# Kernel tuning notes

Measured on AMD Instinct MI355X. Metric: run time of the kernel, lower is better.

## Reference

```python
import jax, jax.numpy as jnp
import numpy as np

LMAX = 8                         # lmax-1 used by s2/so3 irreps
DIMS = [2 * l + 1 for l in range(LMAX + 1)]
S2_OFF = np.cumsum([0] + DIMS).tolist()            # offsets into 81-dim s2 irreps
SO3_OFF = np.cumsum([0] + [d * d for d in DIMS]).tolist()  # offsets into 969-dim so3 irreps
S2_DIM = S2_OFF[-1]              # 81
SO3_DIM = SO3_OFF[-1]            # 969
F_IN = 81                        # multiplicity into S2Conv
F_SO3 = 300
C = 768                          # encoder feature channels
KS = 7                           # encoder feature map / kernel size
B = 8
G_S2 = 48                        # s2 healpix grid rec_level=1
G_ACT = 4096                     # SO3Activation grid points (stand-in for res=20 grid)
G_SO3 = 36864                    # so3 healpix grid rec_level=3


def setup_inputs() -> dict:
    key = jax.random.key(0)
    ks = jax.random.split(key, 7)
    return {
        "x": jax.random.normal(ks[0], (B, C, KS, KS), jnp.float32),
        "F": jax.random.normal(ks[1], (F_IN, S2_DIM * C, KS, KS), jnp.float32) * 0.02,
        "w_s2": jax.random.normal(ks[2], (F_IN, F_SO3, G_S2), jnp.float32) * 0.1,
        "Y": jax.random.normal(ks[3], (G_S2, S2_DIM), jnp.float32),
        "w_so3": jax.random.normal(ks[4], (F_SO3, 1, G_SO3), jnp.float32) * 0.1,
        "D": jax.random.normal(ks[5], (G_SO3, SO3_DIM), jnp.float32),
        "D_act": jax.random.normal(ks[6], (G_ACT, SO3_DIM), jnp.float32),
    }


def _forward(x, F, w_s2, Y, w_so3, D, D_act):
    b = x.shape[0]
    # ---- Induction layer: split expanded R2Conv filter into 768-channel chunks,
    # stack, contract with feature map. g_split: (n=81, c_out=81, C, 7, 7)
    g = jnp.swapaxes(F.reshape(F_IN, S2_DIM, C, KS, KS), 0, 1)
    y = jnp.einsum('ijkhw,akhw->aji', g, x)          # (B, 81, 81): (batch, f_in, s2 irreps)

    # ---- S2Conv: expand kernel into irrep space, per-l block linear (s2 -> so3 irreps)
    psi = jnp.einsum('ni,xyn->xyi', Y, w_s2) / np.sqrt(G_S2)  # (81, 300, 81)
    outs = []
    for l, d in enumerate(DIMS):
        o = S2_OFF[l]
        xl = y[:, :, o:o + d]                        # (B, f_in, 2l+1)
        wl = psi[:, :, o:o + d]                      # (f_in, f_out, mul_out=2l+1)
        ol = jnp.einsum('bfm,fgu->bgum', xl, wl) / np.sqrt(F_IN)
        outs.append(ol.reshape(b, F_SO3, d * d))
    z = jnp.concatenate(outs, axis=-1)               # (B, 300, 969)

    # ---- SO3Activation: to grid, relu, back to irreps
    s = jnp.einsum('bfi,gi->bfg', z, D_act)
    z = jnp.einsum('bfg,gi->bfi', jax.nn.relu(s), D_act) / G_ACT

    # ---- SO3Conv: expand kernel via Wigner-D buffer, per-l block linear (so3 -> so3)
    psi2 = jnp.einsum('ni,xyn->xyi', D, w_so3) / np.sqrt(G_SO3)  # (300, 1, 969)
    outs = []
    for l, d in enumerate(DIMS):
        o = SO3_OFF[l]
        xl = z[:, :, o:o + d * d].reshape(b, F_SO3, d, d)   # (B, f, u, m)
        wl = psi2[:, :, o:o + d * d].reshape(F_SO3, 1, d, d)  # (f, g, v, u)
        ol = jnp.einsum('bfum,fgvu->bgvm', xl, wl) / np.sqrt(F_SO3 * d)
        outs.append(ol.reshape(b, 1, d * d))
    return jnp.concatenate(outs, axis=-1)            # (B, 1, 969)


def reference(x, F, w_s2, Y, w_so3, D, D_act):
    return _forward(x, F, w_s2, Y, w_so3, D, D_act)
```

## Files before the change

kernel.cpp:

```cpp
#include <hip/hip_runtime.h>
#include <hip/hip_bf16.h>
#include <math.h>

#define THREADS 256

constexpr int B_    = 8;
constexpr int C_    = 768;
constexpr int KS_   = 7;
constexpr int F_IN  = 81;
constexpr int F_SO3 = 300;
constexpr int S2_DIM  = 81;
constexpr int SO3_DIM = 969;
constexpr int G_S2  = 48;
constexpr int G_ACT = 4096;
constexpr int G_SO3 = 36864;
constexpr int CKK   = C_ * KS_ * KS_;
constexpr int CKK4  = CKK / 4;
constexpr int NPAIR = F_IN * S2_DIM;

constexpr int D2_SPLIT = 4;
constexpr int E1_SPLIT = 16;
constexpr int F_SPLIT  = 5;

__constant__ int d_S2_OFF[10]  = {0, 1, 4, 9, 16, 25, 36, 49, 64, 81};
__constant__ int d_SO3_OFF[10] = {0, 1, 10, 35, 84, 165, 286, 455, 680, 969};

struct CEnt { unsigned char u, m, so, l; };
struct CLut { CEnt v[992]; };
constexpr CLut make_clut() {
  CLut t{};
  int S2O[10]  = {0, 1, 4, 9, 16, 25, 36, 49, 64, 81};
  int SO3O[10] = {0, 1, 10, 35, 84, 165, 286, 455, 680, 969};
  for (int i = 0; i < 969; ++i) {
    int l = 0;
    while (i >= SO3O[l + 1]) ++l;
    int d = 2 * l + 1, r = i - SO3O[l];
    t.v[i].u  = (unsigned char)(r / d);
    t.v[i].m  = (unsigned char)(r % d);
    t.v[i].so = (unsigned char)S2O[l];
    t.v[i].l  = (unsigned char)l;
  }
  return t;
}
__constant__ CLut g_clut = make_clut();

using short8 = __attribute__((ext_vector_type(8))) short;
using f32x4  = __attribute__((ext_vector_type(4))) float;
using f4v    = __attribute__((ext_vector_type(4))) float;

#define GL16(gp, lp)                                                        \
  __builtin_amdgcn_global_load_lds(                                         \
      (const __attribute__((address_space(1))) void*)(gp),                  \
      (__attribute__((address_space(3))) void*)(lp), 16, 0, 0)

constexpr size_t AL(size_t x) { return (x + 1023) & ~(size_t)1023; }
constexpr size_t O_Y     = 0;
constexpr size_t O_PSI   = O_Y     + AL((size_t)8 * NPAIR * 4);
constexpr size_t O_ZBF   = O_PSI   + AL((size_t)F_IN * F_SO3 * 81 * 4);
constexpr size_t O_DACT  = O_ZBF   + AL((size_t)2432 * 1024 * 2);
constexpr size_t O_DACTT = O_DACT  + AL((size_t)4096 * 1024 * 2);
constexpr size_t O_WSO3  = O_DACTT + AL((size_t)1024 * 4096 * 2);
constexpr size_t O_DT    = O_WSO3  + AL((size_t)384 * 36864 * 2);
constexpr size_t O_SBF   = O_DT    + AL((size_t)1024 * 36864 * 2);
constexpr size_t O_D2P   = O_SBF   + AL((size_t)2432 * 4096 * 2);
constexpr size_t O_E1P   = O_D2P   + AL((size_t)D2_SPLIT * 2432 * 1024 * 4);
constexpr size_t O_PSI2  = O_E1P   + AL((size_t)E1_SPLIT * 384 * 1024 * 4);
constexpr size_t O_SFP   = O_PSI2  + AL((size_t)F_SO3 * SO3_DIM * 4);
constexpr size_t FAST_NEED = O_SFP + AL((size_t)F_SPLIT * 8 * SO3_DIM * 4);

constexpr size_t WS_Y    = 0;
constexpr size_t WS_PSI  = 52488;
constexpr size_t WS_Z    = 2020788;
constexpr size_t WS_S    = 4346388;
constexpr size_t WS_Z2   = 14176788;
constexpr size_t WS_P2P  = 16502388;
constexpr size_t WS_PSI2 = 18827988;

__global__ __launch_bounds__(THREADS, 4) void k_stage_a3(
    const float* __restrict__ Fm, const float* __restrict__ x, float* __restrict__ y) {
  const int p0  = blockIdx.x * 3;
  const int tid = threadIdx.x;
  const f4v* __restrict__ F4 = (const f4v*)Fm;
  const f4v* __restrict__ x4 = (const f4v*)x;

  float acc[3][8];
#pragma unroll
  for (int p = 0; p < 3; ++p)
#pragma unroll
    for (int b = 0; b < 8; ++b) acc[p][b] = 0.f;

  int i = tid;
  for (int it = 0; it < 18; ++it, i += 2 * THREADS) {
    f4v xv0[8], xv1[8];
#pragma unroll
    for (int b = 0; b < 8; ++b) {
      xv0[b] = x4[b * CKK4 + i];
      xv1[b] = x4[b * CKK4 + i + THREADS];
    }
#pragma unroll
    for (int p = 0; p < 3; ++p) {
      f4v fv0 = __builtin_nontemporal_load(&F4[(size_t)(p0 + p) * CKK4 + i]);
      f4v fv1 = __builtin_nontemporal_load(&F4[(size_t)(p0 + p) * CKK4 + i + THREADS]);
#pragma unroll
      for (int b = 0; b < 8; ++b) {
        acc[p][b] += fv0[0] * xv0[b][0] + fv0[1] * xv0[b][1] + fv0[2] * xv0[b][2] + fv0[3] * xv0[b][3];
        acc[p][b] += fv1[0] * xv1[b][0] + fv1[1] * xv1[b][1] + fv1[2] * xv1[b][2] + fv1[3] * xv1[b][3];
      }
    }
  }
  if (i < CKK4) {
    f4v xv0[8];
#pragma unroll
    for (int b = 0; b < 8; ++b) xv0[b] = x4[b * CKK4 + i];
#pragma unroll
    for (int p = 0; p < 3; ++p) {
      f4v fv0 = __builtin_nontemporal_load(&F4[(size_t)(p0 + p) * CKK4 + i]);
#pragma unroll
      for (int b = 0; b < 8; ++b)
        acc[p][b] += fv0[0] * xv0[b][0] + fv0[1] * xv0[b][1] + fv0[2] * xv0[b][2] + fv0[3] * xv0[b][3];
    }
  }

  __shared__ float red[4][24];
  const int lane = tid & 63, wid = tid >> 6;
#pragma unroll
  for (int p = 0; p < 3; ++p) {
#pragma unroll
    for (int b = 0; b < 8; ++b) {
      float v = acc[p][b];
      v += __shfl_down(v, 32);
      v += __shfl_down(v, 16);
      v += __shfl_down(v, 8);
      v += __shfl_down(v, 4);
      v += __shfl_down(v, 2);
      v += __shfl_down(v, 1);
      if (lane == 0) red[wid][p * 8 + b] = v;
    }
  }
  __syncthreads();
  if (tid < 24) {
    float v = red[0][tid] + red[1][tid] + red[2][tid] + red[3][tid];
    int p = tid / 8, b = tid % 8;
    y[(size_t)b * NPAIR + p0 + p] = v;
  }
}

__device__ __forceinline__ void cvt4_body(const float* __restrict__ src,
                                          __hip_bfloat16* __restrict__ dst,
                                          int R, int Cs, int Cp, int blk) {
  size_t e0 = ((size_t)blk * THREADS + threadIdx.x) * 4;
  int r = (int)(e0 / (unsigned)Cp), c = (int)(e0 % (unsigned)Cp);
  __hip_bfloat16 o[4];
#pragma unroll
  for (int j = 0; j < 4; ++j) {
    float v = (r < R && c + j < Cs) ? src[(size_t)r * Cs + c + j] : 0.f;
    o[j] = __float2bfloat16(v);
  }
  *(ushort4*)(&dst[e0]) = *(const ushort4*)o;
}

__device__ __forceinline__ void tr_body(const float* __restrict__ src,
                                        __hip_bfloat16* __restrict__ dst,
                                        int R, int Cs, size_t dstStride, int bx, int by,
                                        char* smemc) {
  float (*tile)[33] = (float(*)[33])smemc;
  const int c0 = bx * 32, r0 = by * 32;
  const int tx = threadIdx.x & 31, ty = threadIdx.x >> 5;
#pragma unroll
  for (int i = 0; i < 32; i += 8) {
    int r = r0 + ty + i, c = c0 + tx;
    tile[ty + i][tx] = (c < Cs) ? src[(size_t)r * Cs + c] : 0.f;
  }
  __syncthreads();
  const int rp = threadIdx.x & 15;
  const int cl = threadIdx.x >> 4;
#pragma unroll
  for (int j = 0; j < 2; ++j) {
    int cc = cl + 16 * j;
    int c  = c0 + cc;
    if (c < Cs) {
      __hip_bfloat16 o[2];
      o[0] = __float2bfloat16(tile[2 * rp][cc]);
      o[1] = __float2bfloat16(tile[2 * rp + 1][cc]);
      *(ushort2*)(&dst[(size_t)c * dstStride + r0 + 2 * rp]) = *(const ushort2*)o;
    }
  }
}

__device__ __forceinline__ void psi_body(const float* __restrict__ w_s2,
                                         const float* __restrict__ Y,
                                         float* __restrict__ psi_t, int blk) {
  int idx = blk * THREADS + threadIdx.x;
  if (idx >= F_IN * F_SO3 * S2_DIM) return;
  int s  = idx % S2_DIM;
  int t1 = idx / S2_DIM;
  int f  = t1 % F_IN;
  int g  = t1 / F_IN;
  const float* w = w_s2 + ((size_t)f * F_SO3 + g) * G_S2;
  float acc = 0.f;
#pragma unroll 8
  for (int n = 0; n < G_S2; ++n) acc += w[n] * Y[n * S2_DIM + s];
  psi_t[idx] = acc * 0.14433756729740643f;
}

constexpr int UB1 = 4096;
constexpr int UB2 = 3968;
constexpr int UB3 = 13824;
constexpr int UB4 = 35712;
constexpr int UB5 = 7689;
constexpr int UB_TOT = UB1 + UB2 + UB3 + UB4 + UB5;

__global__ __launch_bounds__(THREADS) void k_uber(
    const float* __restrict__ D_act, __hip_bfloat16* __restrict__ Dact_bf,
    __hip_bfloat16* __restrict__ DactT_bf,
    const float* __restrict__ w_so3, __hip_bfloat16* __restrict__ wso3_bf,
    const float* __restrict__ D, __hip_bfloat16* __restrict__ DT_bf,
    const float* __restrict__ w_s2, const float* __restrict__ Y, float* __restrict__ psi_t) {
  __shared__ __align__(16) char smem[4352];
  int b = blockIdx.x;
  if (b < UB1) { cvt4_body(D_act, Dact_bf, G_ACT, SO3_DIM, 1024, b); return; }
  b -= UB1;
  if (b < UB2) { tr_body(D_act, DactT_bf, G_ACT, SO3_DIM, 4096, b % 31, b / 31, smem); return; }
  b -= UB2;
  if (b < UB3) { cvt4_body(w_so3, wso3_bf, F_SO3, G_SO3, G_SO3, b); return; }
  b -= UB3;
  if (b < UB4) { tr_body(D, DT_bf, G_SO3, SO3_DIM, 36864, b % 31, b / 31, smem); return; }
  b -= UB4;
  psi_body(w_s2, Y, psi_t, b);
}

__global__ __launch_bounds__(THREADS) void k_stage_c_bf(
    const float* __restrict__ y, const float* __restrict__ psi_t,
    __hip_bfloat16* __restrict__ z) {
  const int b = blockIdx.x / F_SO3;
  const int g = blockIdx.x % F_SO3;
  __shared__ float ybl[NPAIR];
  __shared__ float psl[NPAIR];
  const int tid = threadIdx.x;
  const float* pg = psi_t + (size_t)g * NPAIR;
  for (int t = tid; t < NPAIR; t += THREADS) {
    ybl[t] = y[(size_t)b * NPAIR + t];
    psl[t] = pg[t];
  }
  __syncthreads();
  for (int i = tid; i < 1024; i += THREADS) {
    float acc = 0.f;
    if (i < SO3_DIM) {
      CEnt e = g_clut.v[i];
      int im = e.so + e.m, iu = e.so + e.u;
#pragma unroll 9
      for (int f = 0; f < F_IN; ++f)
        acc += ybl[f * S2_DIM + im] * psl[f * S2_DIM + iu];
      acc *= (1.0f / 9.0f);
    }
    z[((size_t)b * F_SO3 + g) * 1024 + i] = __float2bfloat16(acc);
  }
}

struct GemmDesc {
  const __hip_bfloat16* A;
  const __hip_bfloat16* B;
  void* C;
  int K, kSpan, Ncols;
  float scale;
  size_t splitStride;
  int gx, gy, gz, epi;
};

__device__ __forceinline__ void mfma_nt_body(const GemmDesc g, unsigned lin, char* smem) {
  char* As = smem;
  char* Bs = smem + 16384;

  unsigned nwg = (unsigned)(g.gx * g.gy * g.gz);
  if ((nwg & 7u) == 0u) {
    unsigned q = nwg >> 3;
    lin = (lin & 7u) * q + (lin >> 3);
  }
  const int bxi = (int)(lin % (unsigned)g.gx);
  const unsigned t1 = lin / (unsigned)g.gx;
  const int byi = (int)(t1 % (unsigned)g.gy);
  const int bzi = (int)(t1 / (unsigned)g.gy);

  const int t    = threadIdx.x;
  const int lane = t & 63;
  const int wave = t >> 6;
  const int wr   = wave >> 1, wc = wave & 1;
  const int bm = byi * 128, bn = bxi * 128;
  const int kBegin = bzi * g.kSpan;
  const int kEnd   = kBegin + g.kSpan;

  const char* pA[4];
  const char* pB[4];
  int ldsOff[4];
#pragma unroll
  for (int i = 0; i < 4; ++i) {
    int L   = i * 4096 + t * 16;
    int row = L >> 7;
    int kb  = (L & 127) ^ ((row & 7) << 4);
    pA[i] = (const char*)g.A + ((size_t)(bm + row) * g.K) * 2 + kb;
    pB[i] = (const char*)g.B + ((size_t)(bn + row) * g.K) * 2 + kb;
    ldsOff[i] = L;
  }

  f32x4 acc[4][4] = {};

  for (int k0 = kBegin; k0 < kEnd; k0 += 64) {
    size_t koff = (size_t)k0 * 2;
#pragma unroll
    for (int i = 0; i < 4; ++i) {
      GL16(pA[i] + koff, As + ldsOff[i]);
      GL16(pB[i] + koff, Bs + ldsOff[i]);
    }
    __syncthreads();
#pragma unroll
    for (int kk = 0; kk < 2; ++kk) {
      const int klin = kk * 64 + ((lane >> 4) << 4);
      short8 af[4], bfr[4];
#pragma unroll
      for (int m = 0; m < 4; ++m) {
        int ra = (wr << 6) + (m << 4) + (lane & 15);
        af[m] = *(const short8*)(As + ra * 128 + (klin ^ ((ra & 7) << 4)));
        int rb = (wc << 6) + (m << 4) + (lane & 15);
        bfr[m] = *(const short8*)(Bs + rb * 128 + (klin ^ ((rb & 7) << 4)));
      }
#pragma unroll
      for (int m = 0; m < 4; ++m)
#pragma unroll
        for (int n = 0; n < 4; ++n)
          acc[m][n] = __builtin_amdgcn_mfma_f32_16x16x32_bf16(af[m], bfr[n], acc[m][n], 0, 0, 0);
    }
    __syncthreads();
  }

  const int rbase = bm + (wr << 6) + ((lane >> 4) << 2);
  const int cbase = bn + (wc << 6) + (lane & 15);
  if (g.epi == 0) {
    float* C = (float*)g.C + (size_t)bzi * g.splitStride;
#pragma unroll
    for (int m = 0; m < 4; ++m)
#pragma unroll
      for (int n = 0; n < 4; ++n)
#pragma unroll
        for (int r = 0; r < 4; ++r)
          C[(size_t)(rbase + m * 16 + r) * g.Ncols + (cbase + n * 16)] = acc[m][n][r] * g.scale;
  } else {
    __hip_bfloat16* C = (__hip_bfloat16*)g.C;
#pragma unroll
    for (int m = 0; m < 4; ++m)
#pragma unroll
      for (int n = 0; n < 4; ++n)
#pragma unroll
        for (int r = 0; r < 4; ++r)
          C[(size_t)(rbase + m * 16 + r) * g.Ncols + (cbase + n * 16)] =
              __float2bfloat16(fmaxf(acc[m][n][r], 0.f));
  }
}

__global__ __launch_bounds__(THREADS) void k_mfma_dual(GemmDesc g0, GemmDesc g1, int n0) {
  __shared__ __align__(16) char smem[32768];
  if ((int)blockIdx.x < n0) mfma_nt_body(g0, blockIdx.x, smem);
  else                      mfma_nt_body(g1, blockIdx.x - n0, smem);
}

__global__ __launch_bounds__(THREADS) void k_mfma_reduce(
    GemmDesc g, int n0,
    const float* __restrict__ parts, float* __restrict__ dst, int R, int C,
    size_t rowStride, size_t splitStride, size_t dstStride, int nSplit, float scale) {
  __shared__ __align__(16) char smem[32768];
  if ((int)blockIdx.x < n0) { mfma_nt_body(g, blockIdx.x, smem); return; }
  int idx = (int)(blockIdx.x - n0) * THREADS + threadIdx.x;
  if (idx >= R * C) return;
  int r = idx / C, c = idx % C;
  float a = 0.f;
  for (int s = 0; s < nSplit; ++s) a += parts[(size_t)s * splitStride + (size_t)r * rowStride + c];
  dst[(size_t)r * dstStride + c] = a * scale;
}

__global__ __launch_bounds__(THREADS) void k_stage_f_part(
    const float* __restrict__ d2p, const float* __restrict__ psi2, float* __restrict__ partial) {
  const int b  = blockIdx.x / 9;
  const int l  = blockIdx.x % 9;
  const int sp = blockIdx.y;
  const int d = 2 * l + 1, d2 = d * d;
  const int off = d_SO3_OFF[l];
  constexpr size_t SS = (size_t)2432 * 1024;
  __shared__ float zb[10][289];
  __shared__ float pb[10][289];
  const int tid = threadIdx.x;
  float acc[2] = {0.f, 0.f};
  const int fBeg = sp * (F_SO3 / F_SPLIT), fEnd = fBeg + F_SO3 / F_SPLIT;
  for (int fc = fBeg; fc < fEnd; fc += 10) {
    for (int t = tid; t < 10 * d2; t += THREADS) {
      int fl = t / d2, q = t - fl * d2;
      int f  = fc + fl;
      size_t zi = ((size_t)b * F_SO3 + f) * 1024 + off + q;
      float zv = d2p[zi] + d2p[zi + SS] + d2p[zi + 2 * SS] + d2p[zi + 3 * SS];
      zb[fl][q] = zv * (1.0f / G_ACT);
      pb[fl][q] = psi2[(size_t)f * SO3_DIM + off + q];
    }
    __syncthreads();
#pragma unroll 2
    for (int io = 0; io < 2; ++io) {
      int i = tid + io * THREADS;
      if (i < d2) {
        int v = i / d, m = i - v * d;
        float a = acc[io];
#pragma unroll
        for (int fl = 0; fl < 10; ++fl) {
          float s_ = 0.f;
          for (int u = 0; u < d; ++u)
            s_ += zb[fl][u * d + m] * pb[fl][v * d + u];
          a += s_;
        }
        acc[io] = a;
      }
    }
    __syncthreads();
  }
  for (int io = 0; io < 2; ++io) {
    int i = tid + io * THREADS;
    if (i < d2) partial[((size_t)sp * 8 + b) * SO3_DIM + off + i] = acc[io];
  }
}

__global__ __launch_bounds__(THREADS) void k_stage_f_red(
    const float* __restrict__ partial, float* __restrict__ out) {
  int idx = blockIdx.x * THREADS + threadIdx.x;
  if (idx >= 8 * SO3_DIM) return;
  int b = idx / SO3_DIM, i = idx % SO3_DIM;
  int l = g_clut.v[i].l;
  float a = 0.f;
#pragma unroll
  for (int sp = 0; sp < F_SPLIT; ++sp)
    a += partial[((size_t)sp * 8 + b) * SO3_DIM + i];
  out[(size_t)b * SO3_DIM + i] = a * rsqrtf(300.0f * (float)(2 * l + 1));
}

__global__ __launch_bounds__(THREADS) void k_psi(
    const float* __restrict__ w_s2, const float* __restrict__ Y, float* __restrict__ psi_t) {
  psi_body(w_s2, Y, psi_t, blockIdx.x);
}

__global__ __launch_bounds__(THREADS) void k_stage_c(
    const float* __restrict__ y, const float* __restrict__ psi_t, float* __restrict__ z) {
  const int b = blockIdx.x / F_SO3;
  const int g = blockIdx.x % F_SO3;
  __shared__ float ybl[NPAIR];
  __shared__ float psl[NPAIR];
  const int tid = threadIdx.x;
  const float* pg = psi_t + (size_t)g * NPAIR;
  for (int t = tid; t < NPAIR; t += THREADS) {
    ybl[t] = y[(size_t)b * NPAIR + t];
    psl[t] = pg[t];
  }
  __syncthreads();
  for (int i = tid; i < SO3_DIM; i += THREADS) {
    CEnt e = g_clut.v[i];
    int im = e.so + e.m, iu = e.so + e.u;
    float acc = 0.f;
#pragma unroll 9
    for (int f = 0; f < F_IN; ++f)
      acc += ybl[f * S2_DIM + im] * psl[f * S2_DIM + iu];
    z[((size_t)b * F_SO3 + g) * SO3_DIM + i] = acc * (1.0f / 9.0f);
  }
}

__global__ __launch_bounds__(THREADS) void k_gemm_nt_relu(
    const float* __restrict__ A, const float* __restrict__ Bm, float* __restrict__ Cm,
    int M, int N, int K) {
  __shared__ float As[16][68];
  __shared__ float Bs[16][68];
  const int bm = blockIdx.y * 64, bn = blockIdx.x * 64;
  const int t  = threadIdx.x;
  const int lk = t & 15, lm = t >> 4;
  const int tn = t & 15, tm = t >> 4;
  float acc[4][4] = {};
  for (int k0 = 0; k0 < K; k0 += 16) {
    int gk = k0 + lk;
#pragma unroll
    for (int j = 0; j < 4; ++j) {
      int m  = lm + 16 * j;
      int gm = bm + m;
      As[lk][m] = (gm < M && gk < K) ? A[(size_t)gm * K + gk] : 0.f;
      int gn = bn + m;
      Bs[lk][m] = (gn < N && gk < K) ? Bm[(size_t)gn * K + gk] : 0.f;
    }
    __syncthreads();
#pragma unroll
    for (int k = 0; k < 16; ++k) {
      float4 av = *(const float4*)&As[k][tm * 4];
      float4 bv = *(const float4*)&Bs[k][tn * 4];
      float a[4] = {av.x, av.y, av.z, av.w};
      float bb[4] = {bv.x, bv.y, bv.z, bv.w};
#pragma unroll
      for (int i2 = 0; i2 < 4; ++i2)
#pragma unroll
        for (int j2 = 0; j2 < 4; ++j2)
          acc[i2][j2] += a[i2] * bb[j2];
    }
    __syncthreads();
  }
#pragma unroll
  for (int i2 = 0; i2 < 4; ++i2) {
    int gm = bm + tm * 4 + i2;
    if (gm >= M) continue;
#pragma unroll
    for (int j2 = 0; j2 < 4; ++j2) {
      int gn = bn + tn * 4 + j2;
      if (gn < N) Cm[(size_t)gm * N + gn] = fmaxf(acc[i2][j2], 0.f);
    }
  }
}

__global__ __launch_bounds__(THREADS) void k_gemm_nn(
    const float* __restrict__ A, const float* __restrict__ Bm, float* __restrict__ Cm,
    int M, int N, int K, int kSpan, float scale, size_t cStride) {
  __shared__ float As[16][68];
  __shared__ float Bs[16][68];
  const int bm = blockIdx.y * 64, bn = blockIdx.x * 64;
  const int t   = threadIdx.x;
  const int lk  = t & 15, lm = t >> 4;
  const int ln  = t & 63, lkq = t >> 6;
  const int tn  = t & 15, tm = t >> 4;
  const int kBegin = blockIdx.z * kSpan;
  const int kEnd   = kBegin + kSpan;
  float* C = Cm + (size_t)blockIdx.z * cStride;
  float acc[4][4] = {};
  for (int k0 = kBegin; k0 < kEnd; k0 += 16) {
    {
      int gk = k0 + lk;
#pragma unroll
      for (int j = 0; j < 4; ++j) {
        int m = lm + 16 * j, gm = bm + m;
        As[lk][m] = (gm < M) ? A[(size_t)gm * K + gk] : 0.f;
      }
    }
    {
      int gn = bn + ln;
#pragma unroll
      for (int j = 0; j < 4; ++j) {
        int k = lkq + 4 * j;
        Bs[k][ln] = (gn < N) ? Bm[(size_t)(k0 + k) * N + gn] : 0.f;
      }
    }
    __syncthreads();
#pragma unroll
    for (int k = 0; k < 16; ++k) {
      float4 av = *(const float4*)&As[k][tm * 4];
      float4 bv = *(const float4*)&Bs[k][tn * 4];
      float a[4] = {av.x, av.y, av.z, av.w};
      float bb[4] = {bv.x, bv.y, bv.z, bv.w};
#pragma unroll
      for (int i2 = 0; i2 < 4; ++i2)
#pragma unroll
        for (int j2 = 0; j2 < 4; ++j2)
          acc[i2][j2] += a[i2] * bb[j2];
    }
    __syncthreads();
  }
#pragma unroll
  for (int i2 = 0; i2 < 4; ++i2) {
    int gm = bm + tm * 4 + i2;
    if (gm >= M) continue;
#pragma unroll
    for (int j2 = 0; j2 < 4; ++j2) {
      int gn = bn + tn * 4 + j2;
      if (gn < N) C[(size_t)gm * N + gn] = acc[i2][j2] * scale;
    }
  }
}

__global__ __launch_bounds__(THREADS) void k_reduce_psi2(
    const float* __restrict__ parts, float* __restrict__ psi2) {
  int idx = blockIdx.x * THREADS + threadIdx.x;
  if (idx >= F_SO3 * SO3_DIM) return;
  float acc = 0.f;
#pragma unroll
  for (int s = 0; s < 8; ++s) acc += parts[(size_t)s * (F_SO3 * SO3_DIM) + idx];
  psi2[idx] = acc * (1.0f / 192.0f);
}

__global__ __launch_bounds__(THREADS) void k_stage_f(
    const float* __restrict__ z2, const float* __restrict__ psi2, float* __restrict__ out,
    int zStride) {
  const int b = blockIdx.x / 9;
  const int l = blockIdx.x % 9;
  const int d = 2 * l + 1, d2 = d * d;
  const int off = d_SO3_OFF[l];
  __shared__ float zb[10][289];
  __shared__ float pb[10][289];
  const int tid = threadIdx.x;
  float acc[2] = {0.f, 0.f};
  const float scale = rsqrtf(300.0f * (float)d);
  for (int fc = 0; fc < F_SO3; fc += 10) {
    for (int t = tid; t < 10 * d2; t += THREADS) {
      int fl = t / d2, q = t - fl * d2;
      int f  = fc + fl;
      zb[fl][q] = z2[((size_t)b * F_SO3 + f) * zStride + off + q];
      pb[fl][q] = psi2[(size_t)f * SO3_DIM + off + q];
    }
    __syncthreads();
#pragma unroll 2
    for (int io = 0; io < 2; ++io) {
      int i = tid + io * THREADS;
      if (i < d2) {
        int v = i / d, m = i - v * d;
        float a = acc[io];
#pragma unroll
        for (int fl = 0; fl < 10; ++fl) {
          float s_ = 0.f;
          for (int u = 0; u < d; ++u)
            s_ += zb[fl][u * d + m] * pb[fl][v * d + u];
          a += s_;
        }
        acc[io] = a;
      }
    }
    __syncthreads();
  }
  for (int io = 0; io < 2; ++io) {
    int i = tid + io * THREADS;
    if (i < d2) out[(size_t)b * SO3_DIM + off + i] = acc[io] * scale;
  }
}

extern "C" void kernel_launch(void* const* d_in, const int* in_sizes, int n_in,
                              void* d_out, int out_size, void* d_ws, size_t ws_size,
                              hipStream_t stream) {
  const float* x     = (const float*)d_in[0];
  const float* Fm    = (const float*)d_in[1];
  const float* w_s2  = (const float*)d_in[2];
  const float* Y     = (const float*)d_in[3];
  const float* w_so3 = (const float*)d_in[4];
  const float* D     = (const float*)d_in[5];
  const float* D_act = (const float*)d_in[6];
  float* out = (float*)d_out;

  if (ws_size >= FAST_NEED) {
    char* p = (char*)d_ws;
    float*          y       = (float*)(p + O_Y);
    float*          psi     = (float*)(p + O_PSI);
    __hip_bfloat16* z_bf    = (__hip_bfloat16*)(p + O_ZBF);
    __hip_bfloat16* Dact_bf = (__hip_bfloat16*)(p + O_DACT);
    __hip_bfloat16* DactT_bf= (__hip_bfloat16*)(p + O_DACTT);
    __hip_bfloat16* wso3_bf = (__hip_bfloat16*)(p + O_WSO3);
    __hip_bfloat16* DT_bf   = (__hip_bfloat16*)(p + O_DT);
    __hip_bfloat16* s_bf    = (__hip_bfloat16*)(p + O_SBF);
    float*          d2p     = (float*)(p + O_D2P);
    float*          e1p     = (float*)(p + O_E1P);
    float*          psi2    = (float*)(p + O_PSI2);
    float*          sfp     = (float*)(p + O_SFP);

    k_stage_a3<<<NPAIR / 3, THREADS, 0, stream>>>(Fm, x, y);
    k_uber<<<UB_TOT, THREADS, 0, stream>>>(
        D_act, Dact_bf, DactT_bf, w_so3, wso3_bf, D, DT_bf, w_s2, Y, psi);
    k_stage_c_bf<<<B_ * F_SO3, THREADS, 0, stream>>>(y, psi, z_bf);

    GemmDesc e1{wso3_bf, DT_bf, e1p, G_SO3, G_SO3 / E1_SPLIT, 1024, 1.f,
                (size_t)384 * 1024, 8, 3, E1_SPLIT, 0};
    GemmDesc d1{z_bf, Dact_bf, s_bf, 1024, 1024, 4096, 1.f, 0, 32, 19, 1, 1};
    int nE1 = 8 * 3 * E1_SPLIT;
    int nD1 = 32 * 19;
    k_mfma_dual<<<nE1 + nD1, THREADS, 0, stream>>>(e1, d1, nE1);

    GemmDesc d2{s_bf, DactT_bf, d2p, 4096, 4096 / D2_SPLIT, 1024, 1.f,
                (size_t)2432 * 1024, 8, 19, D2_SPLIT, 0};
    int nD2 = 8 * 19 * D2_SPLIT;
    int nE1r = (F_SO3 * SO3_DIM + THREADS - 1) / THREADS;
    k_mfma_reduce<<<nD2 + nE1r, THREADS, 0, stream>>>(
        d2, nD2, e1p, psi2, F_SO3, SO3_DIM, 1024, (size_t)384 * 1024, SO3_DIM,
        E1_SPLIT, 1.0f / 192.0f);

    k_stage_f_part<<<dim3(B_ * 9, F_SPLIT), THREADS, 0, stream>>>(d2p, psi2, sfp);
    k_stage_f_red<<<(8 * SO3_DIM + THREADS - 1) / THREADS, THREADS, 0, stream>>>(sfp, out);
  } else {
    float* ws  = (float*)d_ws;
    float* y    = ws + WS_Y;
    float* psi  = ws + WS_PSI;
    float* z    = ws + WS_Z;
    float* s    = ws + WS_S;
    float* z2   = ws + WS_Z2;
    float* p2p  = ws + WS_P2P;
    float* psi2 = ws + WS_PSI2;

    k_stage_a3<<<NPAIR / 3, THREADS, 0, stream>>>(Fm, x, y);
    k_psi<<<(F_IN * F_SO3 * S2_DIM + THREADS - 1) / THREADS, THREADS, 0, stream>>>(w_s2, Y, psi);
    k_stage_c<<<B_ * F_SO3, THREADS, 0, stream>>>(y, psi, z);
    k_gemm_nt_relu<<<dim3(G_ACT / 64, (B_ * F_SO3 + 63) / 64), THREADS, 0, stream>>>(
        z, D_act, s, B_ * F_SO3, G_ACT, SO3_DIM);
    k_gemm_nn<<<dim3((SO3_DIM + 63) / 64, (B_ * F_SO3 + 63) / 64, 1), THREADS, 0, stream>>>(
        s, D_act, z2, B_ * F_SO3, SO3_DIM, G_ACT, G_ACT, 1.0f / G_ACT, 0);
    k_gemm_nn<<<dim3((SO3_DIM + 63) / 64, (F_SO3 + 63) / 64, 8), THREADS, 0, stream>>>(
        w_so3, D, p2p, F_SO3, SO3_DIM, G_SO3, G_SO3 / 8, 1.0f, (size_t)F_SO3 * SO3_DIM);
    k_reduce_psi2<<<(F_SO3 * SO3_DIM + THREADS - 1) / THREADS, THREADS, 0, stream>>>(p2p, psi2);
    k_stage_f<<<B_ * 9, THREADS, 0, stream>>>(z2, psi2, out, SO3_DIM);
  }
}
```

Before: 613.8 us.

## Regroup kernel launches so stage A overlaps the E1 GEMM and stage C overlaps its reduction

The launches are re-paired. Stage A (the large F·x contraction) now runs in the same grid as the E1 MFMA GEMM, and stage C runs in the same grid as the E1 split-K reduction. The D1 and D2 GEMMs now each get a dedicated launch. Stage A's unrolled two-iteration loop is also simplified to a single-stride loop. The intent is to overlap the memory-bound stage A with the compute-heavy GEMM and cut the number of launches. The risks are that the combined kernel's large shared memory (52 KB for stage C) lowers occupancy, that the merged kernels use more registers, and that the simpler loop exposes less memory-level parallelism in stage A.

New measurement: 623.7 us. Within noise of the previous version (+1.6%).

```diff
diff --git a/kernel.cpp b/kernel.cpp
--- a/kernel.cpp
+++ b/kernel.cpp
@@ -76,9 +76,10 @@
 constexpr size_t WS_P2P  = 16502388;
 constexpr size_t WS_PSI2 = 18827988;
 
-__global__ __launch_bounds__(THREADS, 4) void k_stage_a3(
-    const float* __restrict__ Fm, const float* __restrict__ x, float* __restrict__ y) {
-  const int p0  = blockIdx.x * 3;
+__device__ __forceinline__ void stage_a_body(
+    const float* __restrict__ Fm, const float* __restrict__ x, float* __restrict__ y,
+    char* smemc, int blk) {
+  const int p0  = blk * 3;
   const int tid = threadIdx.x;
   const f4v* __restrict__ F4 = (const f4v*)Fm;
   const f4v* __restrict__ x4 = (const f4v*)x;
@@ -89,39 +90,20 @@
 #pragma unroll
     for (int b = 0; b < 8; ++b) acc[p][b] = 0.f;
 
-  int i = tid;
-  for (int it = 0; it < 18; ++it, i += 2 * THREADS) {
-    f4v xv0[8], xv1[8];
-#pragma unroll
-    for (int b = 0; b < 8; ++b) {
-      xv0[b] = x4[b * CKK4 + i];
-      xv1[b] = x4[b * CKK4 + i + THREADS];
-    }
+  for (int i = tid; i < CKK4; i += THREADS) {
+    f4v xv[8];
+#pragma unroll
+    for (int b = 0; b < 8; ++b) xv[b] = x4[b * CKK4 + i];
 #pragma unroll
     for (int p = 0; p < 3; ++p) {
-      f4v fv0 = __builtin_nontemporal_load(&F4[(size_t)(p0 + p) * CKK4 + i]);
-      f4v fv1 = __builtin_nontemporal_load(&F4[(size_t)(p0 + p) * CKK4 + i + THREADS]);
-#pragma unroll
-      for (int b = 0; b < 8; ++b) {
-        acc[p][b] += fv0[0] * xv0[b][0] + fv0[1] * xv0[b][1] + fv0[2] * xv0[b][2] + fv0[3] * xv0[b][3];
-        acc[p][b] += fv1[0] * xv1[b][0] + fv1[1] * xv1[b][1] + fv1[2] * xv1[b][2] + fv1[3] * xv1[b][3];
-      }
-    }
-  }
-  if (i < CKK4) {
-    f4v xv0[8];
-#pragma unroll
-    for (int b = 0; b < 8; ++b) xv0[b] = x4[b * CKK4 + i];
-#pragma unroll
-    for (int p = 0; p < 3; ++p) {
-      f4v fv0 = __builtin_nontemporal_load(&F4[(size_t)(p0 + p) * CKK4 + i]);
+      f4v fv = __builtin_nontemporal_load(&F4[(size_t)(p0 + p) * CKK4 + i]);
 #pragma unroll
       for (int b = 0; b < 8; ++b)
-        acc[p][b] += fv0[0] * xv0[b][0] + fv0[1] * xv0[b][1] + fv0[2] * xv0[b][2] + fv0[3] * xv0[b][3];
-    }
-  }
-
-  __shared__ float red[4][24];
+        acc[p][b] += fv[0] * xv[b][0] + fv[1] * xv[b][1] + fv[2] * xv[b][2] + fv[3] * xv[b][3];
+    }
+  }
+
+  float (*red)[24] = (float(*)[24])smemc;
   const int lane = tid & 63, wid = tid >> 6;
 #pragma unroll
   for (int p = 0; p < 3; ++p) {
@@ -229,13 +211,13 @@
   psi_body(w_s2, Y, psi_t, b);
 }
 
-__global__ __launch_bounds__(THREADS) void k_stage_c_bf(
+__device__ __forceinline__ void stage_c_body(
     const float* __restrict__ y, const float* __restrict__ psi_t,
-    __hip_bfloat16* __restrict__ z) {
-  const int b = blockIdx.x / F_SO3;
-  const int g = blockIdx.x % F_SO3;
-  __shared__ float ybl[NPAIR];
-  __shared__ float psl[NPAIR];
+    __hip_bfloat16* __restrict__ z, char* smemc, int blk) {
+  const int b = blk / F_SO3;
+  const int g = blk % F_SO3;
+  float* ybl = (float*)smemc;
+  float* psl = ybl + 6592;
   const int tid = threadIdx.x;
   const float* pg = psi_t + (size_t)g * NPAIR;
   for (int t = tid; t < NPAIR; t += THREADS) {
@@ -356,24 +338,32 @@
   }
 }
 
-__global__ __launch_bounds__(THREADS) void k_mfma_dual(GemmDesc g0, GemmDesc g1, int n0) {
+__global__ __launch_bounds__(THREADS) void k_a_e1(
+    GemmDesc e1, int nE1,
+    const float* __restrict__ Fm, const float* __restrict__ x, float* __restrict__ y) {
   __shared__ __align__(16) char smem[32768];
-  if ((int)blockIdx.x < n0) mfma_nt_body(g0, blockIdx.x, smem);
-  else                      mfma_nt_body(g1, blockIdx.x - n0, smem);
-}
-
-__global__ __launch_bounds__(THREADS) void k_mfma_reduce(
-    GemmDesc g, int n0,
+  if ((int)blockIdx.x < nE1) mfma_nt_body(e1, blockIdx.x, smem);
+  else                       stage_a_body(Fm, x, y, smem, blockIdx.x - nE1);
+}
+
+__global__ __launch_bounds__(THREADS) void k_c_e1r(
+    const float* __restrict__ y, const float* __restrict__ psi_t, __hip_bfloat16* __restrict__ z,
+    int nC,
     const float* __restrict__ parts, float* __restrict__ dst, int R, int C,
     size_t rowStride, size_t splitStride, size_t dstStride, int nSplit, float scale) {
-  __shared__ __align__(16) char smem[32768];
-  if ((int)blockIdx.x < n0) { mfma_nt_body(g, blockIdx.x, smem); return; }
-  int idx = (int)(blockIdx.x - n0) * THREADS + threadIdx.x;
+  __shared__ __align__(16) char smem[52736];
+  if ((int)blockIdx.x < nC) { stage_c_body(y, psi_t, z, smem, blockIdx.x); return; }
+  int idx = (int)(blockIdx.x - nC) * THREADS + threadIdx.x;
   if (idx >= R * C) return;
   int r = idx / C, c = idx % C;
   float a = 0.f;
   for (int s = 0; s < nSplit; ++s) a += parts[(size_t)s * splitStride + (size_t)r * rowStride + c];
   dst[(size_t)r * dstStride + c] = a * scale;
+}
+
+__global__ __launch_bounds__(THREADS) void k_mfma_single(GemmDesc g) {
+  __shared__ __align__(16) char smem[32768];
+  mfma_nt_body(g, blockIdx.x, smem);
 }
 
 __global__ __launch_bounds__(THREADS) void k_stage_f_part(
@@ -436,6 +426,12 @@
   out[(size_t)b * SO3_DIM + i] = a * rsqrtf(300.0f * (float)(2 * l + 1));
 }
 
+__global__ __launch_bounds__(THREADS) void k_stage_a3(
+    const float* __restrict__ Fm, const float* __restrict__ x, float* __restrict__ y) {
+  __shared__ __align__(16) char smem[512];
+  stage_a_body(Fm, x, y, smem, blockIdx.x);
+}
+
 __global__ __launch_bounds__(THREADS) void k_psi(
     const float* __restrict__ w_s2, const float* __restrict__ Y, float* __restrict__ psi_t) {
   psi_body(w_s2, Y, psi_t, blockIdx.x);
@@ -651,25 +647,26 @@
     float*          psi2    = (float*)(p + O_PSI2);
     float*          sfp     = (float*)(p + O_SFP);
 
-    k_stage_a3<<<NPAIR / 3, THREADS, 0, stream>>>(Fm, x, y);
     k_uber<<<UB_TOT, THREADS, 0, stream>>>(
         D_act, Dact_bf, DactT_bf, w_so3, wso3_bf, D, DT_bf, w_s2, Y, psi);
-    k_stage_c_bf<<<B_ * F_SO3, THREADS, 0, stream>>>(y, psi, z_bf);
 
     GemmDesc e1{wso3_bf, DT_bf, e1p, G_SO3, G_SO3 / E1_SPLIT, 1024, 1.f,
                 (size_t)384 * 1024, 8, 3, E1_SPLIT, 0};
+    int nE1 = 8 * 3 * E1_SPLIT;
+    k_a_e1<<<nE1 + NPAIR / 3, THREADS, 0, stream>>>(e1, nE1, Fm, x, y);
+
+    int nC = B_ * F_SO3;
+    int nE1r = (F_SO3 * SO3_DIM + THREADS - 1) / THREADS;
+    k_c_e1r<<<nC + nE1r, THREADS, 0, stream>>>(
+        y, psi, z_bf, nC, e1p, psi2, F_SO3, SO3_DIM, 1024, (size_t)384 * 1024,
+        SO3_DIM, E1_SPLIT, 1.0f / 192.0f);
+
     GemmDesc d1{z_bf, Dact_bf, s_bf, 1024, 1024, 4096, 1.f, 0, 32, 19, 1, 1};
-    int nE1 = 8 * 3 * E1_SPLIT;
-    int nD1 = 32 * 19;
-    k_mfma_dual<<<nE1 + nD1, THREADS, 0, stream>>>(e1, d1, nE1);
+    k_mfma_single<<<32 * 19, THREADS, 0, stream>>>(d1);
 
     GemmDesc d2{s_bf, DactT_bf, d2p, 4096, 4096 / D2_SPLIT, 1024, 1.f,
                 (size_t)2432 * 1024, 8, 19, D2_SPLIT, 0};
-    int nD2 = 8 * 19 * D2_SPLIT;
-    int nE1r = (F_SO3 * SO3_DIM + THREADS - 1) / THREADS;
-    k_mfma_reduce<<<nD2 + nE1r, THREADS, 0, stream>>>(
-        d2, nD2, e1p, psi2, F_SO3, SO3_DIM, 1024, (size_t)384 * 1024, SO3_DIM,
-        E1_SPLIT, 1.0f / 192.0f);
+    k_mfma_single<<<8 * 19 * D2_SPLIT, THREADS, 0, stream>>>(d2);
 
     k_stage_f_part<<<dim3(B_ * 9, F_SPLIT), THREADS, 0, stream>>>(d2p, psi2, sfp);
     k_stage_f_red<<<(8 * SO3_DIM + THREADS - 1) / THREADS, THREADS, 0, stream>>>(sfp, out);
```

## Double split-K factors and factor stage-A body into a reusable device function

Applied to the files above, without the earlier changes.

Raises the split-K partition counts for the D2 and E1 GEMM stages from 4/16 to 8/32, so more blocks run concurrently and each covers a shorter reduction. The downstream reduction now loops over D2_SPLIT partials. Stage A's dot-product loop is simplified to a single strided loop without manual 2x unrolling, and its body is moved into an inline device function that takes shared memory from the caller, apparently so it can later be fused with other stages. More partials mean more workspace traffic and more reduction work.

After: 612.2 us. Within noise of the previous version (-0.3%).

```diff
diff --git a/kernel.cpp b/kernel.cpp
--- a/kernel.cpp
+++ b/kernel.cpp
@@ -18,8 +18,8 @@
 constexpr int CKK4  = CKK / 4;
 constexpr int NPAIR = F_IN * S2_DIM;
 
-constexpr int D2_SPLIT = 4;
-constexpr int E1_SPLIT = 16;
+constexpr int D2_SPLIT = 8;
+constexpr int E1_SPLIT = 32;
 constexpr int F_SPLIT  = 5;
 
 __constant__ int d_S2_OFF[10]  = {0, 1, 4, 9, 16, 25, 36, 49, 64, 81};
@@ -76,9 +76,10 @@
 constexpr size_t WS_P2P  = 16502388;
 constexpr size_t WS_PSI2 = 18827988;
 
-__global__ __launch_bounds__(THREADS, 4) void k_stage_a3(
-    const float* __restrict__ Fm, const float* __restrict__ x, float* __restrict__ y) {
-  const int p0  = blockIdx.x * 3;
+__device__ __forceinline__ void stage_a_body(
+    const float* __restrict__ Fm, const float* __restrict__ x, float* __restrict__ y,
+    char* smemc, int blk) {
+  const int p0  = blk * 3;
   const int tid = threadIdx.x;
   const f4v* __restrict__ F4 = (const f4v*)Fm;
   const f4v* __restrict__ x4 = (const f4v*)x;
@@ -89,39 +90,20 @@
 #pragma unroll
     for (int b = 0; b < 8; ++b) acc[p][b] = 0.f;
 
-  int i = tid;
-  for (int it = 0; it < 18; ++it, i += 2 * THREADS) {
-    f4v xv0[8], xv1[8];
-#pragma unroll
-    for (int b = 0; b < 8; ++b) {
-      xv0[b] = x4[b * CKK4 + i];
-      xv1[b] = x4[b * CKK4 + i + THREADS];
-    }
+  for (int i = tid; i < CKK4; i += THREADS) {
+    f4v xv[8];
+#pragma unroll
+    for (int b = 0; b < 8; ++b) xv[b] = x4[b * CKK4 + i];
 #pragma unroll
     for (int p = 0; p < 3; ++p) {
-      f4v fv0 = __builtin_nontemporal_load(&F4[(size_t)(p0 + p) * CKK4 + i]);
-      f4v fv1 = __builtin_nontemporal_load(&F4[(size_t)(p0 + p) * CKK4 + i + THREADS]);
-#pragma unroll
-      for (int b = 0; b < 8; ++b) {
-        acc[p][b] += fv0[0] * xv0[b][0] + fv0[1] * xv0[b][1] + fv0[2] * xv0[b][2] + fv0[3] * xv0[b][3];
-        acc[p][b] += fv1[0] * xv1[b][0] + fv1[1] * xv1[b][1] + fv1[2] * xv1[b][2] + fv1[3] * xv1[b][3];
-      }
-    }
-  }
-  if (i < CKK4) {
-    f4v xv0[8];
-#pragma unroll
-    for (int b = 0; b < 8; ++b) xv0[b] = x4[b * CKK4 + i];
-#pragma unroll
-    for (int p = 0; p < 3; ++p) {
-      f4v fv0 = __builtin_nontemporal_load(&F4[(size_t)(p0 + p) * CKK4 + i]);
+      f4v fv = __builtin_nontemporal_load(&F4[(size_t)(p0 + p) * CKK4 + i]);
 #pragma unroll
       for (int b = 0; b < 8; ++b)
-        acc[p][b] += fv0[0] * xv0[b][0] + fv0[1] * xv0[b][1] + fv0[2] * xv0[b][2] + fv0[3] * xv0[b][3];
-    }
-  }
-
-  __shared__ float red[4][24];
+        acc[p][b] += fv[0] * xv[b][0] + fv[1] * xv[b][1] + fv[2] * xv[b][2] + fv[3] * xv[b][3];
+    }
+  }
+
+  float (*red)[24] = (float(*)[24])smemc;
   const int lane = tid & 63, wid = tid >> 6;
 #pragma unroll
   for (int p = 0; p < 3; ++p) {
@@ -394,7 +376,9 @@
       int fl = t / d2, q = t - fl * d2;
       int f  = fc + fl;
       size_t zi = ((size_t)b * F_SO3 + f) * 1024 + off + q;
-      float zv = d2p[zi] + d2p[zi + SS] + d2p[zi + 2 * SS] + d2p[zi + 3 * SS];
+      float zv = 0.f;
+#pragma unroll
+      for (int s = 0; s < D2_SPLIT; ++s) zv += d2p[zi + (size_t)s * SS];
       zb[fl][q] = zv * (1.0f / G_ACT);
       pb[fl][q] = psi2[(size_t)f * SO3_DIM + off + q];
     }
@@ -434,6 +418,12 @@
   for (int sp = 0; sp < F_SPLIT; ++sp)
     a += partial[((size_t)sp * 8 + b) * SO3_DIM + i];
   out[(size_t)b * SO3_DIM + i] = a * rsqrtf(300.0f * (float)(2 * l + 1));
+}
+
+__global__ __launch_bounds__(THREADS) void k_stage_a3(
+    const float* __restrict__ Fm, const float* __restrict__ x, float* __restrict__ y) {
+  __shared__ __align__(16) char smem[512];
+  stage_a_body(Fm, x, y, smem, blockIdx.x);
 }
 
 __global__ __launch_bounds__(THREADS) void k_psi(
```
